# Kernel optimization log

Hardware: AMD Instinct MI355X
Metric: run time of the kernel (lower is better)

## Reference

```python
import jax, jax.numpy as jnp
import numpy as np

H = 16
D_MODEL = 1024
D_K = D_MODEL // H


def setup_inputs() -> dict:
    key = jax.random.key(0)
    ks = jax.random.split(key, 11)
    B, S = 2, 2048
    scale = 1.0 / np.sqrt(D_MODEL)
    inp = {
        "query": jax.random.normal(ks[0], (B, S, D_MODEL), dtype=jnp.float32),
        "key": jax.random.normal(ks[1], (B, S, D_MODEL), dtype=jnp.float32),
        "value": jax.random.normal(ks[2], (B, S, D_MODEL), dtype=jnp.float32),
        "Wq": jax.random.normal(ks[3], (D_MODEL, D_MODEL), dtype=jnp.float32) * scale,
        "bq": jnp.zeros((D_MODEL,), dtype=jnp.float32),
        "Wk": jax.random.normal(ks[4], (D_MODEL, D_MODEL), dtype=jnp.float32) * scale,
        "bk": jnp.zeros((D_MODEL,), dtype=jnp.float32),
        "Wv": jax.random.normal(ks[5], (D_MODEL, D_MODEL), dtype=jnp.float32) * scale,
        "bv": jnp.zeros((D_MODEL,), dtype=jnp.float32),
        "Wo": jax.random.normal(ks[6], (D_MODEL, D_MODEL), dtype=jnp.float32) * scale,
        "bo": jnp.zeros((D_MODEL,), dtype=jnp.float32),
    }
    return inp


def _mha(query, key, value, Wq, bq, Wk, bk, Wv, bv, Wo, bo):
    B, S, _ = query.shape
    # linear projections (torch nn.Linear: x @ W.T + b)
    q = query @ Wq.T + bq
    k = key @ Wk.T + bk
    v = value @ Wv.T + bv
    # split heads: [B, S, D] -> [B, H, S, d_k]
    q = q.reshape(B, S, H, D_K).transpose(0, 2, 1, 3)
    k = k.reshape(B, S, H, D_K).transpose(0, 2, 1, 3)
    v = v.reshape(B, S, H, D_K).transpose(0, 2, 1, 3)
    # scaled dot-product attention with manual stable softmax
    scores = jnp.einsum("bhqd,bhkd->bhqk", q, k) / jnp.sqrt(jnp.float32(D_K))
    stable = scores - jnp.max(scores, axis=-1, keepdims=True)
    e = jnp.exp(stable)
    attn = e / jnp.sum(e, axis=-1, keepdims=True)
    ctx = jnp.einsum("bhqk,bhkd->bhqd", attn, v)
    # merge heads and final projection
    ctx = ctx.transpose(0, 2, 1, 3).reshape(B, S, H * D_K)
    return ctx @ Wo.T + bo


def reference(query, key, value, Wq, bq, Wk, bk, Wv, bv, Wo, bo):
    return _mha(query, key, value, Wq, bq, Wk, bk, Wv, bv, Wo, bo)
```

## Files before the change

kernel.cpp:

```cpp
#include <hip/hip_runtime.h>


#define S_LEN 2048
#define BATCH 2
#define DM    1024
#define NH    16
#define DKH   64
#define BS    (BATCH * S_LEN)

typedef _Float16 f16x8 __attribute__((ext_vector_type(8)));
typedef _Float16 f16x4 __attribute__((ext_vector_type(4)));
typedef _Float16 f16x2 __attribute__((ext_vector_type(2)));
typedef __fp16   h16x2 __attribute__((ext_vector_type(2)));
typedef float    f32x4 __attribute__((ext_vector_type(4)));

__device__ __forceinline__ f16x2 pk_f16(float a, float b) {
  h16x2 r = __builtin_amdgcn_cvt_pkrtz(a, b);
  return __builtin_bit_cast(f16x2, r);
}

__device__ __forceinline__ void gld16(const void* g, void* l) {
  __builtin_amdgcn_global_load_lds(
      (const __attribute__((address_space(1))) void*)g,
      (__attribute__((address_space(3))) void*)l, 16, 0, 0);
}

__device__ __forceinline__ float fast_exp2(float x) {
#if __has_builtin(__builtin_amdgcn_exp2f)
  return __builtin_amdgcn_exp2f(x);
#else
  return exp2f(x);
#endif
}

__global__ __launch_bounds__(256) void cvt_all(
    const float* __restrict__ q, const float* __restrict__ k, const float* __restrict__ v,
    const float* __restrict__ wq, const float* __restrict__ wk,
    const float* __restrict__ wv, const float* __restrict__ wo,
    _Float16* __restrict__ xq, _Float16* __restrict__ xk, _Float16* __restrict__ xv,
    _Float16* __restrict__ w16)
{
  const int y = blockIdx.y;
  const float* src; _Float16* dst; int n;
  if (y == 0)      { src = q;  dst = xq; n = BS * DM; }
  else if (y == 1) { src = k;  dst = xk; n = BS * DM; }
  else if (y == 2) { src = v;  dst = xv; n = BS * DM; }
  else {
    src = (y == 3) ? wq : ((y == 4) ? wk : ((y == 5) ? wv : wo));
    dst = w16 + (size_t)(y - 3) * (DM * DM);
    n = DM * DM;
  }
  int i0 = (blockIdx.x * 256 + threadIdx.x) * 4;
  if (i0 < n) {
    float4 f = *(const float4*)(src + i0);
    f16x2 lo = pk_f16(f.x, f.y);
    f16x2 hi = pk_f16(f.z, f.w);
    f16x4 h; h[0] = lo[0]; h[1] = lo[1]; h[2] = hi[0]; h[3] = hi[1];
    *(f16x4*)(dst + i0) = h;
  }
}

template <typename OUT_T>
__device__ __forceinline__ void gemm_core(
    const _Float16* __restrict__ A, const _Float16* __restrict__ W,
    const float* __restrict__ bias, OUT_T* __restrict__ out, float oscale)
{
  const int tid  = threadIdx.x;
  const int l    = tid & 63;
  const int wv   = tid >> 6;
  const int c    = l & 15, quad = l >> 4;
  const int m0   = blockIdx.y * 128, n0 = blockIdx.x * 128;
  const int wm   = wv & 1, wn = wv >> 1;
  __shared__ _Float16 sA[128 * 32];
  __shared__ _Float16 sB[128 * 32];

  const int s0 = tid, s1 = tid + 256;
  const int r0 = s0 >> 2, g0 = (s0 & 3) ^ ((s0 >> 3) & 3);
  const int r1 = s1 >> 2, g1 = (s1 & 3) ^ ((s1 >> 3) & 3);
  const _Float16* ga0 = A + (size_t)(m0 + r0) * DM + g0 * 8;
  const _Float16* ga1 = A + (size_t)(m0 + r1) * DM + g1 * 8;
  const _Float16* gb0 = W + (size_t)(n0 + r0) * DM + g0 * 8;
  const _Float16* gb1 = W + (size_t)(n0 + r1) * DM + g1 * 8;
  const int sw = (c >> 1) & 3;

  f32x4 acc[4][4] = {};
  for (int k0 = 0; k0 < DM; k0 += 32) {
    __syncthreads();
    gld16(ga0 + k0, sA + s0 * 8);
    gld16(ga1 + k0, sA + s1 * 8);
    gld16(gb0 + k0, sB + s0 * 8);
    gld16(gb1 + k0, sB + s1 * 8);
    __syncthreads();
    f16x8 af[4], bf[4];
#pragma unroll
    for (int i = 0; i < 4; ++i)
      af[i] = *(const f16x8*)&sA[(wm * 64 + i * 16 + c) * 32 + (quad ^ sw) * 8];
#pragma unroll
    for (int j = 0; j < 4; ++j)
      bf[j] = *(const f16x8*)&sB[(wn * 64 + j * 16 + c) * 32 + (quad ^ sw) * 8];
#pragma unroll
    for (int i = 0; i < 4; ++i)
#pragma unroll
      for (int j = 0; j < 4; ++j)
        acc[i][j] = __builtin_amdgcn_mfma_f32_16x16x32_f16(af[i], bf[j], acc[i][j], 0, 0, 0);
  }
#pragma unroll
  for (int j = 0; j < 4; ++j) {
    int col = n0 + wn * 64 + j * 16 + c;
    float bb = bias[col];
#pragma unroll
    for (int i = 0; i < 4; ++i) {
      int row = m0 + wm * 64 + i * 16 + quad * 4;
#pragma unroll
      for (int r = 0; r < 4; ++r) {
        float vv = (acc[i][j][r] + bb) * oscale;
        out[(size_t)(row + r) * DM + col] = (OUT_T)vv;
      }
    }
  }
}

#define SC_Q (0.125f * 1.44269504088896340736f)

__global__ __launch_bounds__(256) void proj3(
    const _Float16* __restrict__ xq, const _Float16* __restrict__ xk,
    const _Float16* __restrict__ xv, const _Float16* __restrict__ w16,
    const float* __restrict__ bq, const float* __restrict__ bk, const float* __restrict__ bv,
    _Float16* __restrict__ Q, _Float16* __restrict__ K, _Float16* __restrict__ V)
{
  const int z = blockIdx.z;
  const _Float16* A    = (z == 0) ? xq : ((z == 1) ? xk : xv);
  const _Float16* W    = w16 + (size_t)z * (DM * DM);
  const float*    bias = (z == 0) ? bq : ((z == 1) ? bk : bv);
  _Float16*       out  = (z == 0) ? Q : ((z == 1) ? K : V);
  const float     os   = (z == 0) ? SC_Q : 1.0f;
  gemm_core<_Float16>(A, W, bias, out, os);
}

__global__ __launch_bounds__(256) void out_gemm(
    const _Float16* __restrict__ ctx, const _Float16* __restrict__ wo,
    const float* __restrict__ bo, float* __restrict__ out)
{
  gemm_core<float>(ctx, wo, bo, out, 1.0f);
}

__global__ __launch_bounds__(256) void vtrans(const _Float16* __restrict__ V,
                                              _Float16* __restrict__ Vt)
{
  const int tid = threadIdx.x;
  const int s0  = blockIdx.x * 64;
  const int bh  = blockIdx.y;
  const int b   = bh >> 4, h = bh & 15;
  __shared__ _Float16 t[64 * 68];
  const _Float16* Vg = V + ((size_t)(b * S_LEN + s0)) * DM + h * DKH;
#pragma unroll
  for (int p = 0; p < 2; ++p) {
    int cc = tid + p * 256;
    int r = cc >> 3, off = (cc & 7) << 3;
    f16x8 vv = *(const f16x8*)(Vg + (size_t)r * DM + off);
    f16x4 lo, hi;
    lo.x = vv[0]; lo.y = vv[1]; lo.z = vv[2]; lo.w = vv[3];
    hi.x = vv[4]; hi.y = vv[5]; hi.z = vv[6]; hi.w = vv[7];
    *(f16x4*)&t[r * 68 + off]     = lo;
    *(f16x4*)&t[r * 68 + off + 4] = hi;
  }
  __syncthreads();
  const int cpos = tid & 63, dbase = tid >> 6;
  _Float16* Og = Vt + ((size_t)bh * DKH) * S_LEN + s0 + cpos;
#pragma unroll
  for (int i = 0; i < 16; ++i) {
    int d = dbase + i * 4;
    Og[(size_t)d * S_LEN] = t[cpos * 68 + d];
  }
}

#define APP 72
__global__ __launch_bounds__(256) void attn(
    const _Float16* __restrict__ Q, const _Float16* __restrict__ K,
    const _Float16* __restrict__ Vt, _Float16* __restrict__ ctx)
{
  const int tid = threadIdx.x;
  const int l   = tid & 63, wv = tid >> 6;
  const int c   = l & 15, quad = l >> 4;
  const int q0  = blockIdx.x * 64;
  const int bh  = blockIdx.y;
  const int b   = bh >> 4, h = bh & 15;
  __shared__ _Float16 sK[64 * 64];
  __shared__ _Float16 sV[64 * 64];
  __shared__ _Float16 sP[4][16 * APP];

  const _Float16* Qg = Q + ((size_t)(b * S_LEN + q0 + wv * 16 + c)) * DM + h * DKH;
  f16x8 qf[2];
  qf[0] = *(const f16x8*)(Qg + quad * 8);
  qf[1] = *(const f16x8*)(Qg + 32 + quad * 8);

  f32x4 o[4] = {};
  float l_part = 0.f;

  const _Float16* Kg0 = K + ((size_t)b * S_LEN) * DM + h * DKH;
  const _Float16* Vg0 = Vt + ((size_t)bh * DKH) * S_LEN;

  const int sa = tid,      ra = sa >> 3, ba = (sa & 7) ^ (ra & 7);
  const int sb = tid + 256, rb = sb >> 3, bb = (sb & 7) ^ (rb & 7);
  const _Float16* gKa = Kg0 + (size_t)ra * DM + ba * 8;
  const _Float16* gKb = Kg0 + (size_t)rb * DM + bb * 8;
  const _Float16* gVa = Vg0 + (size_t)ra * S_LEN + ba * 8;
  const _Float16* gVb = Vg0 + (size_t)rb * S_LEN + bb * 8;
  const int cx = c & 7;

  for (int kt = 0; kt < S_LEN / 64; ++kt) {
    const int k0 = kt * 64;
    __syncthreads();
    gld16(gKa + (size_t)k0 * DM, sK + sa * 8);
    gld16(gKb + (size_t)k0 * DM, sK + sb * 8);
    gld16(gVa + k0,              sV + sa * 8);
    gld16(gVb + k0,              sV + sb * 8);
    __syncthreads();

    f32x4 sAcc[4] = {};
#pragma unroll
    for (int ks = 0; ks < 2; ++ks)
#pragma unroll
      for (int nt = 0; nt < 4; ++nt) {
        f16x8 kf = *(const f16x8*)&sK[(nt * 16 + c) * 64 + ((ks * 4 + quad) ^ cx) * 8];
        sAcc[nt] = __builtin_amdgcn_mfma_f32_16x16x32_f16(kf, qf[ks], sAcc[nt], 0, 0, 0);
      }

#pragma unroll
    for (int nt = 0; nt < 4; ++nt) {
      float p0 = fast_exp2(sAcc[nt][0]);
      float p1 = fast_exp2(sAcc[nt][1]);
      float p2 = fast_exp2(sAcc[nt][2]);
      float p3 = fast_exp2(sAcc[nt][3]);
      l_part += (p0 + p1) + (p2 + p3);
      f16x2 lo = pk_f16(p0, p1);
      f16x2 hi = pk_f16(p2, p3);
      f16x4 pk; pk[0] = lo[0]; pk[1] = lo[1]; pk[2] = hi[0]; pk[3] = hi[1];
      *(f16x4*)&sP[wv][c * APP + nt * 16 + quad * 4] = pk;
    }

#pragma unroll
    for (int ks = 0; ks < 2; ++ks) {
      f16x8 af = *(const f16x8*)&sP[wv][c * APP + ks * 32 + quad * 8];
#pragma unroll
      for (int nt = 0; nt < 4; ++nt) {
        f16x8 bf = *(const f16x8*)&sV[(nt * 16 + c) * 64 + ((ks * 4 + quad) ^ cx) * 8];
        o[nt] = __builtin_amdgcn_mfma_f32_16x16x32_f16(af, bf, o[nt], 0, 0, 0);
      }
    }
  }

  l_part += __shfl_xor(l_part, 16);
  l_part += __shfl_xor(l_part, 32);

  _Float16* Og = ctx + ((size_t)(b * S_LEN + q0 + wv * 16 + quad * 4)) * DM + h * DKH;
#pragma unroll
  for (int j = 0; j < 4; ++j) {
    float s = __shfl(l_part, quad * 4 + j, 64);
    float inv = 1.0f / s;
#pragma unroll
    for (int nt = 0; nt < 4; ++nt)
      Og[(size_t)j * DM + nt * 16 + c] = (_Float16)(o[nt][j] * inv);
  }
}

extern "C" void kernel_launch(void* const* d_in, const int* in_sizes, int n_in,
                              void* d_out, int out_size, void* d_ws, size_t ws_size,
                              hipStream_t stream)
{
  (void)in_sizes; (void)n_in; (void)out_size; (void)ws_size;
  const float* q  = (const float*)d_in[0];
  const float* k  = (const float*)d_in[1];
  const float* v  = (const float*)d_in[2];
  const float* wq = (const float*)d_in[3];
  const float* bq = (const float*)d_in[4];
  const float* wk = (const float*)d_in[5];
  const float* bk = (const float*)d_in[6];
  const float* wv = (const float*)d_in[7];
  const float* bv = (const float*)d_in[8];
  const float* wo = (const float*)d_in[9];
  const float* bo = (const float*)d_in[10];

  char* ws = (char*)d_ws;
  _Float16* XQ  = (_Float16*)(ws);
  _Float16* XK  = (_Float16*)(ws + (8u  << 20));
  _Float16* XV  = (_Float16*)(ws + (16u << 20));
  _Float16* W16 = (_Float16*)(ws + (24u << 20));
  _Float16* Qp  = (_Float16*)(ws + (32u << 20));
  _Float16* Kp  = (_Float16*)(ws + (40u << 20));
  _Float16* Vp  = (_Float16*)(ws + (48u << 20));
  _Float16* VT  = XK;
  _Float16* CTX = XQ;
  float* out = (float*)d_out;

  cvt_all<<<dim3(4096, 7), 256, 0, stream>>>(q, k, v, wq, wk, wv, wo, XQ, XK, XV, W16);
  proj3<<<dim3(8, 32, 3), 256, 0, stream>>>(XQ, XK, XV, W16, bq, bk, bv, Qp, Kp, Vp);
  vtrans<<<dim3(32, 32), 256, 0, stream>>>(Vp, VT);
  attn<<<dim3(32, 32), 256, 0, stream>>>(Qp, Kp, VT, CTX);
  out_gemm<<<dim3(8, 32), 256, 0, stream>>>(CTX, W16 + (size_t)3 * DM * DM, bo, out);
}
```

Baseline: 248.2 us.

## Double GEMM K-tile to 64 and process 128 queries per attention block

```diff
diff --git a/kernel.cpp b/kernel.cpp
--- a/kernel.cpp
+++ b/kernel.cpp
@@ -71,38 +71,42 @@
   const int c    = l & 15, quad = l >> 4;
   const int m0   = blockIdx.y * 128, n0 = blockIdx.x * 128;
   const int wm   = wv & 1, wn = wv >> 1;
-  __shared__ _Float16 sA[128 * 32];
-  __shared__ _Float16 sB[128 * 32];
-
-  const int s0 = tid, s1 = tid + 256;
-  const int r0 = s0 >> 2, g0 = (s0 & 3) ^ ((s0 >> 3) & 3);
-  const int r1 = s1 >> 2, g1 = (s1 & 3) ^ ((s1 >> 3) & 3);
-  const _Float16* ga0 = A + (size_t)(m0 + r0) * DM + g0 * 8;
-  const _Float16* ga1 = A + (size_t)(m0 + r1) * DM + g1 * 8;
-  const _Float16* gb0 = W + (size_t)(n0 + r0) * DM + g0 * 8;
-  const _Float16* gb1 = W + (size_t)(n0 + r1) * DM + g1 * 8;
-  const int sw = (c >> 1) & 3;
+  __shared__ _Float16 sA[128 * 64];
+  __shared__ _Float16 sB[128 * 64];
+
+  const _Float16* gA[4]; const _Float16* gB[4];
+#pragma unroll
+  for (int p = 0; p < 4; ++p) {
+    int s = tid + p * 256, r = s >> 3, g = (s & 7) ^ (r & 7);
+    gA[p] = A + (size_t)(m0 + r) * DM + g * 8;
+    gB[p] = W + (size_t)(n0 + r) * DM + g * 8;
+  }
+  const int cx = c & 7;
 
   f32x4 acc[4][4] = {};
-  for (int k0 = 0; k0 < DM; k0 += 32) {
+  for (int k0 = 0; k0 < DM; k0 += 64) {
     __syncthreads();
-    gld16(ga0 + k0, sA + s0 * 8);
-    gld16(ga1 + k0, sA + s1 * 8);
-    gld16(gb0 + k0, sB + s0 * 8);
-    gld16(gb1 + k0, sB + s1 * 8);
+#pragma unroll
+    for (int p = 0; p < 4; ++p) {
+      gld16(gA[p] + k0, sA + (tid + p * 256) * 8);
+      gld16(gB[p] + k0, sB + (tid + p * 256) * 8);
+    }
     __syncthreads();
-    f16x8 af[4], bf[4];
-#pragma unroll
-    for (int i = 0; i < 4; ++i)
-      af[i] = *(const f16x8*)&sA[(wm * 64 + i * 16 + c) * 32 + (quad ^ sw) * 8];
-#pragma unroll
-    for (int j = 0; j < 4; ++j)
-      bf[j] = *(const f16x8*)&sB[(wn * 64 + j * 16 + c) * 32 + (quad ^ sw) * 8];
-#pragma unroll
-    for (int i = 0; i < 4; ++i)
+#pragma unroll
+    for (int ks = 0; ks < 2; ++ks) {
+      f16x8 af[4], bf[4];
+#pragma unroll
+      for (int i = 0; i < 4; ++i)
+        af[i] = *(const f16x8*)&sA[(wm * 64 + i * 16 + c) * 64 + ((ks * 4 + quad) ^ cx) * 8];
 #pragma unroll
       for (int j = 0; j < 4; ++j)
-        acc[i][j] = __builtin_amdgcn_mfma_f32_16x16x32_f16(af[i], bf[j], acc[i][j], 0, 0, 0);
+        bf[j] = *(const f16x8*)&sB[(wn * 64 + j * 16 + c) * 64 + ((ks * 4 + quad) ^ cx) * 8];
+#pragma unroll
+      for (int i = 0; i < 4; ++i)
+#pragma unroll
+        for (int j = 0; j < 4; ++j)
+          acc[i][j] = __builtin_amdgcn_mfma_f32_16x16x32_f16(af[i], bf[j], acc[i][j], 0, 0, 0);
+    }
   }
 #pragma unroll
   for (int j = 0; j < 4; ++j) {
@@ -182,20 +186,23 @@
   const int tid = threadIdx.x;
   const int l   = tid & 63, wv = tid >> 6;
   const int c   = l & 15, quad = l >> 4;
-  const int q0  = blockIdx.x * 64;
+  const int q0  = blockIdx.x * 128;
   const int bh  = blockIdx.y;
   const int b   = bh >> 4, h = bh & 15;
   __shared__ _Float16 sK[64 * 64];
   __shared__ _Float16 sV[64 * 64];
-  __shared__ _Float16 sP[4][16 * APP];
-
-  const _Float16* Qg = Q + ((size_t)(b * S_LEN + q0 + wv * 16 + c)) * DM + h * DKH;
-  f16x8 qf[2];
-  qf[0] = *(const f16x8*)(Qg + quad * 8);
-  qf[1] = *(const f16x8*)(Qg + 32 + quad * 8);
-
-  f32x4 o[4] = {};
-  float l_part = 0.f;
+  __shared__ _Float16 sP[4][32 * APP];
+
+  f16x8 qf[2][2];
+#pragma unroll
+  for (int qc = 0; qc < 2; ++qc) {
+    const _Float16* Qg = Q + ((size_t)(b * S_LEN + q0 + wv * 32 + qc * 16 + c)) * DM + h * DKH;
+    qf[qc][0] = *(const f16x8*)(Qg + quad * 8);
+    qf[qc][1] = *(const f16x8*)(Qg + 32 + quad * 8);
+  }
+
+  f32x4 o[2][4] = {};
+  float l_part[2] = {};
 
   const _Float16* Kg0 = K + ((size_t)b * S_LEN) * DM + h * DKH;
   const _Float16* Vg0 = Vt + ((size_t)bh * DKH) * S_LEN;
@@ -217,50 +224,62 @@
     gld16(gVb + k0,              sV + sb * 8);
     __syncthreads();
 
-    f32x4 sAcc[4] = {};
+    f32x4 sAcc[2][4] = {};
 #pragma unroll
     for (int ks = 0; ks < 2; ++ks)
 #pragma unroll
       for (int nt = 0; nt < 4; ++nt) {
         f16x8 kf = *(const f16x8*)&sK[(nt * 16 + c) * 64 + ((ks * 4 + quad) ^ cx) * 8];
-        sAcc[nt] = __builtin_amdgcn_mfma_f32_16x16x32_f16(kf, qf[ks], sAcc[nt], 0, 0, 0);
+#pragma unroll
+        for (int qc = 0; qc < 2; ++qc)
+          sAcc[qc][nt] = __builtin_amdgcn_mfma_f32_16x16x32_f16(kf, qf[qc][ks], sAcc[qc][nt], 0, 0, 0);
       }
 
 #pragma unroll
-    for (int nt = 0; nt < 4; ++nt) {
-      float p0 = fast_exp2(sAcc[nt][0]);
-      float p1 = fast_exp2(sAcc[nt][1]);
-      float p2 = fast_exp2(sAcc[nt][2]);
-      float p3 = fast_exp2(sAcc[nt][3]);
-      l_part += (p0 + p1) + (p2 + p3);
-      f16x2 lo = pk_f16(p0, p1);
-      f16x2 hi = pk_f16(p2, p3);
-      f16x4 pk; pk[0] = lo[0]; pk[1] = lo[1]; pk[2] = hi[0]; pk[3] = hi[1];
-      *(f16x4*)&sP[wv][c * APP + nt * 16 + quad * 4] = pk;
-    }
+    for (int qc = 0; qc < 2; ++qc)
+#pragma unroll
+      for (int nt = 0; nt < 4; ++nt) {
+        float p0 = fast_exp2(sAcc[qc][nt][0]);
+        float p1 = fast_exp2(sAcc[qc][nt][1]);
+        float p2 = fast_exp2(sAcc[qc][nt][2]);
+        float p3 = fast_exp2(sAcc[qc][nt][3]);
+        l_part[qc] += (p0 + p1) + (p2 + p3);
+        f16x2 lo = pk_f16(p0, p1);
+        f16x2 hi = pk_f16(p2, p3);
+        f16x4 pk; pk[0] = lo[0]; pk[1] = lo[1]; pk[2] = hi[0]; pk[3] = hi[1];
+        *(f16x4*)&sP[wv][(qc * 16 + c) * APP + nt * 16 + quad * 4] = pk;
+      }
 
 #pragma unroll
     for (int ks = 0; ks < 2; ++ks) {
-      f16x8 af = *(const f16x8*)&sP[wv][c * APP + ks * 32 + quad * 8];
-#pragma unroll
-      for (int nt = 0; nt < 4; ++nt) {
-        f16x8 bf = *(const f16x8*)&sV[(nt * 16 + c) * 64 + ((ks * 4 + quad) ^ cx) * 8];
-        o[nt] = __builtin_amdgcn_mfma_f32_16x16x32_f16(af, bf, o[nt], 0, 0, 0);
+      f16x8 bf[4];
+#pragma unroll
+      for (int nt = 0; nt < 4; ++nt)
+        bf[nt] = *(const f16x8*)&sV[(nt * 16 + c) * 64 + ((ks * 4 + quad) ^ cx) * 8];
+#pragma unroll
+      for (int qc = 0; qc < 2; ++qc) {
+        f16x8 af = *(const f16x8*)&sP[wv][(qc * 16 + c) * APP + ks * 32 + quad * 8];
+#pragma unroll
+        for (int nt = 0; nt < 4; ++nt)
+          o[qc][nt] = __builtin_amdgcn_mfma_f32_16x16x32_f16(af, bf[nt], o[qc][nt], 0, 0, 0);
       }
     }
   }
 
-  l_part += __shfl_xor(l_part, 16);
-  l_part += __shfl_xor(l_part, 32);
-
-  _Float16* Og = ctx + ((size_t)(b * S_LEN + q0 + wv * 16 + quad * 4)) * DM + h * DKH;
-#pragma unroll
-  for (int j = 0; j < 4; ++j) {
-    float s = __shfl(l_part, quad * 4 + j, 64);
-    float inv = 1.0f / s;
-#pragma unroll
-    for (int nt = 0; nt < 4; ++nt)
-      Og[(size_t)j * DM + nt * 16 + c] = (_Float16)(o[nt][j] * inv);
+#pragma unroll
+  for (int qc = 0; qc < 2; ++qc) {
+    float lp = l_part[qc];
+    lp += __shfl_xor(lp, 16);
+    lp += __shfl_xor(lp, 32);
+    _Float16* Og = ctx + ((size_t)(b * S_LEN + q0 + wv * 32 + qc * 16 + quad * 4)) * DM + h * DKH;
+#pragma unroll
+    for (int j = 0; j < 4; ++j) {
+      float s = __shfl(lp, quad * 4 + j, 64);
+      float inv = 1.0f / s;
+#pragma unroll
+      for (int nt = 0; nt < 4; ++nt)
+        Og[(size_t)j * DM + nt * 16 + c] = (_Float16)(o[qc][nt][j] * inv);
+    }
   }
 }
 
@@ -296,6 +315,6 @@
   cvt_all<<<dim3(4096, 7), 256, 0, stream>>>(q, k, v, wq, wk, wv, wo, XQ, XK, XV, W16);
   proj3<<<dim3(8, 32, 3), 256, 0, stream>>>(XQ, XK, XV, W16, bq, bk, bv, Qp, Kp, Vp);
   vtrans<<<dim3(32, 32), 256, 0, stream>>>(Vp, VT);
-  attn<<<dim3(32, 32), 256, 0, stream>>>(Qp, Kp, VT, CTX);
+  attn<<<dim3(16, 32), 256, 0, stream>>>(Qp, Kp, VT, CTX);
   out_gemm<<<dim3(8, 32), 256, 0, stream>>>(CTX, W16 + (size_t)3 * DM * DM, bo, out);
 }
```

Measured after the change: 251.6 us. No clear change (+1.4%).
